# Performance work log

Hardware: AMD Instinct MI355X
Metric: run time of the kernel (lower is better)

Reference implementation:

```python
import jax, jax.numpy as jnp
import numpy as np
import math

B, L, DIM = 2, 2048, 1024
NUM_HEADS, QUANTUM_HEADS, CHUNK = 16, 2, 64
HD = DIM // NUM_HEADS  # 64 == CHUNK (required by the original broadcast)
TH = NUM_HEADS - QUANTUM_HEADS
STEPS = 2048
LN_EPS = 1e-5


def setup_inputs() -> dict:
    key = jax.random.key(0)
    ks = jax.random.split(key, 12)
    inp = {
        'x': jax.random.normal(ks[0], (B, L, DIM), dtype=jnp.float32),
        # to_quantum_state: Linear(HD, 2HD) + LayerNorm(2HD) + Tanh
        'wq1': jax.random.normal(ks[1], (HD, 2 * HD), dtype=jnp.float32) * 0.05,
        'bq1': jnp.zeros((2 * HD,), dtype=jnp.float32),
        'ln_g': jnp.ones((2 * HD,), dtype=jnp.float32),
        'ln_b': jnp.zeros((2 * HD,), dtype=jnp.float32),
        'phase_shifts': jax.random.normal(ks[2], (QUANTUM_HEADS,), dtype=jnp.float32) * 0.02,
        'freqs': jax.random.normal(ks[3], (QUANTUM_HEADS,), dtype=jnp.float32) * 0.02,
        # traditional heads: q/k/v projections, no bias
        'wq': jax.random.normal(ks[4], (DIM, TH * HD), dtype=jnp.float32) * 0.02,
        'wk': jax.random.normal(ks[5], (DIM, TH * HD), dtype=jnp.float32) * 0.02,
        'wv': jax.random.normal(ks[6], (DIM, TH * HD), dtype=jnp.float32) * 0.02,
        # output projection
        'wo': jax.random.normal(ks[7], (DIM, DIM), dtype=jnp.float32) * 0.02,
        'bo': jnp.zeros((DIM,), dtype=jnp.float32),
    }
    return inp


def _quantum_state(t, wq1, bq1, ln_g, ln_b):
    # Linear -> LayerNorm -> Tanh; split into (amp, phase)
    h = t @ wq1 + bq1
    mu = h.mean(-1, keepdims=True)
    var = ((h - mu) ** 2).mean(-1, keepdims=True)
    h = (h - mu) * jax.lax.rsqrt(var + LN_EPS) * ln_g + ln_b
    h = jnp.tanh(h)
    return h[..., :HD], h[..., HD:]


def reference(x, wq1, bq1, ln_g, ln_b, phase_shifts, freqs, wq, wk, wv, wo, bo):
    two_pi = 2.0 * math.pi
    angles = jnp.linspace(0.0, two_pi, STEPS)  # torch.linspace is endpoint-inclusive
    cos_table = jnp.cos(angles)
    inv_sqrt_hd = 1.0 / math.sqrt(HD)
    nc = L // CHUNK

    quantum_outs = []
    for h in range(QUANTUM_HEADS):
        xh = x[..., h * HD:(h + 1) * HD]                       # [B,L,HD]
        amp, phase = _quantum_state(xh, wq1, bq1, ln_g, ln_b)  # each [B,L,HD]
        qa = amp.reshape(B, nc, CHUNK, HD)
        qp = phase.reshape(B, nc, CHUNK, HD)
        # keys/values are truncated to the FIRST `chunk` tokens (original quirk)
        ka = amp[:, :CHUNK]        # [B,CHUNK,HD]
        kp = phase[:, :CHUNK]
        v = xh[:, :CHUNK]
        # phase_diff[b,c,i,j] = qp[b,c,i,j] - kp[b,j,i]  (needs CHUNK == HD)
        pd = (qp - jnp.swapaxes(kp, -1, -2)[:, None]) * freqs[h] + phase_shifts[h]
        idx = jnp.mod(pd / two_pi * STEPS, STEPS).astype(jnp.int32)  # in [0, STEPS)
        interference = cos_table[idx]                          # [B,nc,CHUNK,CHUNK]
        scores = jnp.einsum('bcih,bjh->bcij', qa, ka) * interference
        attn = jax.nn.softmax(scores * inv_sqrt_hd, axis=-1)
        out = jnp.einsum('bcij,bjh->bcih', attn, v).reshape(B, L, HD)
        quantum_outs.append(out)

    # traditional multi-head attention on full x
    q = (x @ wq).reshape(B, L, TH, HD)
    k = (x @ wk).reshape(B, L, TH, HD)
    vv = (x @ wv).reshape(B, L, TH, HD)
    scores = jnp.einsum('bqhd,bkhd->bhqk', q, k) * inv_sqrt_hd
    attn = jax.nn.softmax(scores, axis=-1)
    trad = jnp.einsum('bhqk,bkhd->bqhd', attn, vv).reshape(B, L, TH * HD)

    out = jnp.concatenate(quantum_outs + [trad], axis=-1)  # [B,L,DIM]
    return out @ wo + bo
```

## Files before the change

kernel.cpp:

```cpp
#include <hip/hip_runtime.h>
#include <hip/hip_bf16.h>
#include <math.h>

#define B_ 2
#define L_ 2048
#define DIM_ 1024
#define HD_ 64
#define TH_ 14
#define TWO_PI_F 6.28318530717958647692f
#define QSCALE_F 0.1803368801111204f

typedef __bf16 bf16_t;
typedef __bf16 bf16x8 __attribute__((ext_vector_type(8)));
typedef __bf16 bf16x4 __attribute__((ext_vector_type(4)));
typedef float f32x4 __attribute__((ext_vector_type(4)));
typedef float f32x16 __attribute__((ext_vector_type(16)));
typedef unsigned int u32x2 __attribute__((ext_vector_type(2)));

static __device__ __forceinline__ bf16_t f2b(float f) { return (bf16_t)f; }

static __device__ __forceinline__ float fexp2(float x) {
#if __has_builtin(__builtin_amdgcn_exp2f)
  return __builtin_amdgcn_exp2f(x);
#else
  return exp2f(x);
#endif
}

static __device__ __forceinline__ unsigned int cvtpk(float a, float b) {
  unsigned int r;
  asm("v_cvt_pk_bf16_f32 %0, %1, %2" : "=v"(r) : "v"(a), "v"(b));
  return r;
}

static __device__ __forceinline__ void gl16(const bf16_t* g, bf16_t* l) {
  __builtin_amdgcn_global_load_lds(
      (const __attribute__((address_space(1))) void*)g,
      (__attribute__((address_space(3))) void*)l, 16, 0, 0);
}

static __device__ __forceinline__ void swap32(unsigned int& a, unsigned int& b) {
#if __has_builtin(__builtin_amdgcn_permlane32_swap)
  u32x2 r = __builtin_amdgcn_permlane32_swap(a, b, false, false);
  a = r[0];
  b = r[1];
#else
  const int l = (int)(threadIdx.x & 63);
  unsigned int bp_a = (unsigned int)__builtin_amdgcn_ds_bpermute((l ^ 32) << 2, (int)a);
  unsigned int bp_b = (unsigned int)__builtin_amdgcn_ds_bpermute((l ^ 32) << 2, (int)b);
  unsigned int na = (l < 32) ? a : bp_b;
  unsigned int nb = (l < 32) ? bp_a : b;
  a = na;
  b = nb;
#endif
}

__global__ __launch_bounds__(256)
void k_prep(const float* __restrict__ x, const float* __restrict__ wq1,
            const float* __restrict__ bq1, const float* __restrict__ ln_g,
            const float* __restrict__ ln_b, const float* __restrict__ wq,
            const float* __restrict__ wk, const float* __restrict__ wv,
            const float* __restrict__ wo, bf16_t* __restrict__ xb,
            bf16_t* __restrict__ wt_qkv, bf16_t* __restrict__ wt_o,
            bf16_t* __restrict__ amp_b, float* __restrict__ phase) {
  __shared__ float tile[32][33];
  const int t = threadIdx.x;
  const int bid = blockIdx.x;
  if (bid < 4096) {
    const int i = bid * 256 + t;
    const float4 v4 = ((const float4*)x)[i];
    bf16x4 o = {f2b(v4.x), f2b(v4.y), f2b(v4.z), f2b(v4.w)};
    *(bf16x4*)(xb + 4 * (size_t)i) = o;
  } else if (bid < 7808) {
    const float* W;
    bf16_t* Wt;
    int N, kt, nt;
    if (bid < 6784) {
      int r = bid - 4096;
      const int which = r / 896;
      r -= which * 896;
      W = (which == 0) ? wq : (which == 1) ? wk : wv;
      Wt = wt_qkv + (size_t)which * 896 * 1024;
      N = 896;
      kt = r & 31;
      nt = r >> 5;
    } else {
      const int r = bid - 6784;
      W = wo;
      Wt = wt_o;
      N = 1024;
      kt = r & 31;
      nt = r >> 5;
    }
    const int tx = t & 31, ty = t >> 5;
    const int k0 = kt * 32, n0 = nt * 32;
    #pragma unroll
    for (int i = 0; i < 4; ++i)
      tile[ty + 8 * i][tx] = W[(size_t)(k0 + ty + 8 * i) * N + n0 + tx];
    __syncthreads();
    #pragma unroll
    for (int i = 0; i < 4; ++i)
      Wt[(size_t)(n0 + ty + 8 * i) * 1024 + k0 + tx] = f2b(tile[tx][ty + 8 * i]);
  } else {
    const int gw = ((bid - 7808) * 256 + t) >> 6;
    const int lane = t & 63;
    const int h = gw >> 12;
    const int bl = gw & 4095;
    const float xv = x[(size_t)bl * DIM_ + h * HD_ + lane];
    float acc0 = bq1[lane];
    float acc1 = bq1[64 + lane];
    #pragma unroll 16
    for (int kk = 0; kk < 64; ++kk) {
      const float xk = __shfl(xv, kk, 64);
      acc0 = fmaf(xk, wq1[kk * 128 + lane], acc0);
      acc1 = fmaf(xk, wq1[kk * 128 + 64 + lane], acc1);
    }
    float s = acc0 + acc1;
    #pragma unroll
    for (int off = 32; off > 0; off >>= 1) s += __shfl_xor(s, off, 64);
    const float mu = s * (1.0f / 128.0f);
    const float d0 = acc0 - mu, d1 = acc1 - mu;
    float vsum = d0 * d0 + d1 * d1;
    #pragma unroll
    for (int off = 32; off > 0; off >>= 1) vsum += __shfl_xor(vsum, off, 64);
    const float rstd = rsqrtf(vsum * (1.0f / 128.0f) + 1e-5f);
    const float av = tanhf(d0 * rstd * ln_g[lane] + ln_b[lane]);
    const float pv = tanhf(d1 * rstd * ln_g[64 + lane] + ln_b[64 + lane]);
    const size_t o = ((size_t)h * (B_ * L_) + bl) * HD_ + lane;
    amp_b[o] = f2b(av);
    phase[o] = pv;
  }
}

__global__ __launch_bounds__(256)
void k_mm1q(const bf16_t* __restrict__ A, const bf16_t* __restrict__ Wt,
            bf16_t* __restrict__ qb, bf16_t* __restrict__ kb, bf16_t* __restrict__ vb,
            const bf16_t* __restrict__ amp_b, const float* __restrict__ phase,
            const float* __restrict__ shifts, const float* __restrict__ freqs,
            bf16_t* __restrict__ catb) {
  __shared__ char smem[32768];
  const int t = threadIdx.x;
  const int lane = t & 63, w = t >> 6;
  const int bid = blockIdx.x;
  const int v = (bid & 7) * 100 + (bid >> 3);
  if (v < 672) {
    bf16_t* Asm = (bf16_t*)smem;
    bf16_t* Bsm = (bf16_t*)(smem + 16384);
    const int wm = w >> 1, wn = w & 1;
    const int l15 = lane & 15, g = lane >> 4;
    const int m0 = (v & 31) * 128;
    const int n0 = (v >> 5) * 128;
    f32x4 acc[4][4] = {};
    for (int k0 = 0; k0 < 1024; k0 += 64) {
      __syncthreads();
      #pragma unroll
      for (int qc = 0; qc < 4; ++qc) {
        const int idx = t + 256 * qc;
        const int r = idx >> 3, cb = idx & 7;
        const int c = (cb ^ (r & 7)) * 8;
        gl16(A + (size_t)(m0 + r) * 1024 + k0 + c, Asm + w * 512 + qc * 2048);
        gl16(Wt + (size_t)(n0 + r) * 1024 + k0 + c, Bsm + w * 512 + qc * 2048);
      }
      __syncthreads();
      #pragma unroll
      for (int ks = 0; ks < 2; ++ks) {
        bf16x8 af[4], bfr[4];
        #pragma unroll
        for (int mi = 0; mi < 4; ++mi) {
          const int row = wm * 64 + mi * 16 + l15;
          af[mi] = *(const bf16x8*)((char*)Asm + row * 128 + (((ks * 4 + g) ^ (row & 7)) << 4));
        }
        #pragma unroll
        for (int ni = 0; ni < 4; ++ni) {
          const int row = wn * 64 + ni * 16 + l15;
          bfr[ni] = *(const bf16x8*)((char*)Bsm + row * 128 + (((ks * 4 + g) ^ (row & 7)) << 4));
        }
        #pragma unroll
        for (int mi = 0; mi < 4; ++mi)
          #pragma unroll
          for (int ni = 0; ni < 4; ++ni)
            acc[mi][ni] = __builtin_amdgcn_mfma_f32_16x16x32_bf16(bfr[ni], af[mi], acc[mi][ni], 0, 0, 0);
      }
    }
    const int n0w = n0 + wn * 64;
    const int which = (n0 >= 1792) ? 2 : (n0 >= 896) ? 1 : 0;
    #pragma unroll
    for (int mi = 0; mi < 4; ++mi) {
      const int m = m0 + wm * 64 + mi * 16 + (lane & 15);
      const int bsel = m >> 11, ll = m & 2047;
      #pragma unroll
      for (int ni = 0; ni < 4; ++ni) {
        const int nb = n0w + ni * 16 + (lane >> 4) * 4;
        const int nn = nb - which * 896;
        const int head = nn >> 6, hd = nn & 63;
        if (which == 2) {
          #pragma unroll
          for (int r = 0; r < 4; ++r)
            vb[(((size_t)bsel * TH_ + head) * HD_ + hd + r) * L_ + ll] = f2b(acc[mi][ni][r]);
        } else {
          const float sc = (which == 0) ? QSCALE_F : 1.0f;
          bf16_t* dst = (which == 0) ? qb : kb;
          bf16x4 pk;
          #pragma unroll
          for (int r = 0; r < 4; ++r) pk[r] = f2b(acc[mi][ni][r] * sc);
          *(bf16x4*)(dst + (((size_t)bsel * TH_ + head) * L_ + ll) * HD_ + hd) = pk;
        }
      }
    }
  } else {
    bf16_t* Kam = (bf16_t*)smem;
    bf16_t* Vt  = (bf16_t*)(smem + 8192);
    bf16_t* Ps  = (bf16_t*)(smem + 16384);
    const int l15 = lane & 15, g = lane >> 4;
    const int qv = v - 672;
    const int c = qv & 31;
    const int hb = qv >> 5;
    const int b = hb & 1;
    const int h = hb >> 1;
    const size_t abase = ((size_t)h * B_ + b) * L_ * HD_;

    {
      const int r0 = t >> 3, cb0 = t & 7;
      const int r1 = r0 + 32;
      gl16(amp_b + abase + r0 * 64 + (cb0 ^ (r0 & 7)) * 8, Kam + w * 512);
      gl16(amp_b + abase + r1 * 64 + (cb0 ^ (r1 & 7)) * 8, Kam + w * 512 + 2048);
    }
    {
      const int vj = t >> 2;
      const int vd0 = (t & 3) * 16;
      const bf16x8 va = *(const bf16x8*)(A + ((size_t)b * L_ + vj) * DIM_ + h * 64 + vd0);
      const bf16x8 vb2 = *(const bf16x8*)(A + ((size_t)b * L_ + vj) * DIM_ + h * 64 + vd0 + 8);
      #pragma unroll
      for (int e = 0; e < 8; ++e) {
        int d = vd0 + e;
        *(bf16_t*)((char*)Vt + d * 128 + (((vj >> 3) ^ (d & 7)) << 4) + (vj & 7) * 2) = va[e];
        d = vd0 + 8 + e;
        *(bf16_t*)((char*)Vt + d * 128 + (((vj >> 3) ^ (d & 7)) << 4) + (vj & 7) * 2) = vb2[e];
      }
    }
    __syncthreads();

    bf16x8 qf[2];
    {
      const size_t ro = abase + (size_t)(c * 64 + 16 * w + l15) * 64 + g * 8;
      qf[0] = *(const bf16x8*)(amp_b + ro);
      qf[1] = *(const bf16x8*)(amp_b + ro + 32);
    }
    f32x4 s[4] = {};
    #pragma unroll
    for (int ks = 0; ks < 2; ++ks) {
      #pragma unroll
      for (int nt = 0; nt < 4; ++nt) {
        const int jr = nt * 16 + l15;
        const bf16x8 kf = *(const bf16x8*)((char*)Kam + jr * 128 + (((ks * 4 + g) ^ (jr & 7)) << 4));
        s[nt] = __builtin_amdgcn_mfma_f32_16x16x32_bf16(qf[ks], kf, s[nt], 0, 0, 0);
      }
    }
    const float freq = freqs[h], shift = shifts[h];
    char* PsW = (char*)Ps + w * 2048;
    float l_acc[4];
    #pragma unroll
    for (int r = 0; r < 4; ++r) {
      const int i_loc = 16 * w + 4 * g + r;
      const float* qrow = phase + abase + (size_t)(c * 64 + i_loc) * 64;
      const float* krow = phase + abase + i_loc;
      const int row = g * 4 + r;
      float ls = 0.0f;
      #pragma unroll
      for (int nt = 0; nt < 4; ++nt) {
        const int j = nt * 16 + l15;
        const float qp = qrow[j];
        const float kp = krow[j * 64];
        const float pd = (qp - kp) * freq + shift;
        const float t1 = pd * (2048.0f / TWO_PI_F);
        float mm = fmodf(t1, 2048.0f);
        if (mm < 0.0f) mm += 2048.0f;
        int idx = (int)mm;
        idx = idx > 2047 ? 2047 : idx;
        const float interf = cosf((float)idx * (TWO_PI_F / 2047.0f));
        const float sc = s[nt][r] * interf * 0.125f;
        const float e = expf(sc);
        ls += e;
        *(bf16_t*)(PsW + row * 128 + (((j >> 3) ^ (row & 7)) << 4) + (j & 7) * 2) = f2b(e);
      }
      #pragma unroll
      for (int off = 1; off < 16; off <<= 1) ls += __shfl_xor(ls, off, 64);
      l_acc[r] = ls;
    }
    f32x4 o[4] = {};
    #pragma unroll
    for (int ks = 0; ks < 2; ++ks) {
      const bf16x8 pa = *(const bf16x8*)(PsW + l15 * 128 + (((ks * 4 + g) ^ (l15 & 7)) << 4));
      #pragma unroll
      for (int nt = 0; nt < 4; ++nt) {
        const int dr = nt * 16 + l15;
        const bf16x8 vf = *(const bf16x8*)((char*)Vt + dr * 128 + (((ks * 4 + g) ^ (dr & 7)) << 4));
        o[nt] = __builtin_amdgcn_mfma_f32_16x16x32_bf16(pa, vf, o[nt], 0, 0, 0);
      }
    }
    #pragma unroll
    for (int r = 0; r < 4; ++r) {
      const float inv = 1.0f / l_acc[r];
      const int qrow = c * 64 + 16 * w + g * 4 + r;
      #pragma unroll
      for (int nt = 0; nt < 4; ++nt)
        catb[((size_t)b * L_ + qrow) * DIM_ + h * 64 + nt * 16 + l15] = f2b(o[nt][r] * inv);
    }
  }
}

__global__ __launch_bounds__(256)
void k_mm0(const bf16_t* __restrict__ A, const bf16_t* __restrict__ Wt,
           const float* __restrict__ bias, float* __restrict__ outf) {
  __shared__ bf16_t Asm[128 * 64];
  __shared__ bf16_t Bsm[128 * 64];
  const int t = threadIdx.x;
  const int lane = t & 63, w = t >> 6;
  const int wm = w >> 1, wn = w & 1;
  const int l15 = lane & 15, g = lane >> 4;
  const int bid = blockIdx.x;
  const int v = (bid & 7) * 32 + (bid >> 3);
  const int m0 = (v & 31) * 128;
  const int n0 = (v >> 5) * 128;
  f32x4 acc[4][4] = {};
  for (int k0 = 0; k0 < 1024; k0 += 64) {
    __syncthreads();
    #pragma unroll
    for (int qc = 0; qc < 4; ++qc) {
      const int idx = t + 256 * qc;
      const int r = idx >> 3, cb = idx & 7;
      const int c = (cb ^ (r & 7)) * 8;
      gl16(A + (size_t)(m0 + r) * 1024 + k0 + c, Asm + w * 512 + qc * 2048);
      gl16(Wt + (size_t)(n0 + r) * 1024 + k0 + c, Bsm + w * 512 + qc * 2048);
    }
    __syncthreads();
    #pragma unroll
    for (int ks = 0; ks < 2; ++ks) {
      bf16x8 af[4], bfr[4];
      #pragma unroll
      for (int mi = 0; mi < 4; ++mi) {
        const int row = wm * 64 + mi * 16 + l15;
        af[mi] = *(const bf16x8*)((char*)Asm + row * 128 + (((ks * 4 + g) ^ (row & 7)) << 4));
      }
      #pragma unroll
      for (int ni = 0; ni < 4; ++ni) {
        const int row = wn * 64 + ni * 16 + l15;
        bfr[ni] = *(const bf16x8*)((char*)Bsm + row * 128 + (((ks * 4 + g) ^ (row & 7)) << 4));
      }
      #pragma unroll
      for (int mi = 0; mi < 4; ++mi)
        #pragma unroll
        for (int ni = 0; ni < 4; ++ni)
          acc[mi][ni] = __builtin_amdgcn_mfma_f32_16x16x32_bf16(bfr[ni], af[mi], acc[mi][ni], 0, 0, 0);
    }
  }
  #pragma unroll
  for (int mi = 0; mi < 4; ++mi) {
    const int m = m0 + wm * 64 + mi * 16 + l15;
    #pragma unroll
    for (int ni = 0; ni < 4; ++ni) {
      const int nb = n0 + wn * 64 + ni * 16 + g * 4;
      const float4 bv = *(const float4*)&bias[nb];
      float4 r4;
      r4.x = acc[mi][ni][0] + bv.x;
      r4.y = acc[mi][ni][1] + bv.y;
      r4.z = acc[mi][ni][2] + bv.z;
      r4.w = acc[mi][ni][3] + bv.w;
      *(float4*)&outf[(size_t)m * 1024 + nb] = r4;
    }
  }
}

__global__ __launch_bounds__(256)
void k_flash2(const bf16_t* __restrict__ qg, const bf16_t* __restrict__ kg,
              const bf16_t* __restrict__ vt, bf16_t* __restrict__ catb) {
  __shared__ bf16_t Ks2[2][64 * 64];
  __shared__ bf16_t Vs2[2][64 * 64];
  const int t = threadIdx.x;
  const int lane = t & 63, w = t >> 6;
  const int l31 = lane & 31, hi = lane >> 5;
  int bid = blockIdx.x;
  bid = (bid & 7) * 56 + (bid >> 3);
  const int qblk = bid & 15, bh = bid >> 4;
  const int head = bh % TH_, b = bh / TH_;
  const size_t base = (size_t)bh * (L_ * HD_);
  const int q = qblk * 128 + w * 32 + l31;
  const int r0 = t >> 3, cb0 = t & 7;
  const int r1 = r0 + 32;
  const int c0 = (cb0 ^ (r0 & 7)) * 8;
  const int c1 = (cb0 ^ (r1 & 7)) * 8;
  const int ubase = w * 512;

  bf16x8 qf[4];
  #pragma unroll
  for (int slot = 0; slot < 4; ++slot)
    qf[slot] = *(const bf16x8*)(qg + base + (size_t)q * 64 + 16 * slot + 8 * hi);

  f32x16 oT[2] = {};
  float l_acc = 0.0f;

  {
    const bf16_t* ksrc = kg + base;
    const bf16_t* vsrc = vt + base;
    gl16(ksrc + r0 * 64 + c0, &Ks2[0][ubase]);
    gl16(ksrc + r1 * 64 + c1, &Ks2[0][ubase + 2048]);
    gl16(vsrc + (size_t)r0 * L_ + c0, &Vs2[0][ubase]);
    gl16(vsrc + (size_t)r1 * L_ + c1, &Vs2[0][ubase + 2048]);
  }
  for (int kt = 0; kt < 32; ++kt) {
    const int cur = kt & 1;
    if (kt < 31) {
      const bf16_t* ksrc = kg + base + (size_t)(kt + 1) * 64 * 64;
      const bf16_t* vsrc = vt + base + (kt + 1) * 64;
      bf16_t* kd = &Ks2[cur ^ 1][0];
      bf16_t* vd = &Vs2[cur ^ 1][0];
      gl16(ksrc + r0 * 64 + c0, kd + ubase);
      gl16(ksrc + r1 * 64 + c1, kd + ubase + 2048);
      gl16(vsrc + (size_t)r0 * L_ + c0, vd + ubase);
      gl16(vsrc + (size_t)r1 * L_ + c1, vd + ubase + 2048);
      asm volatile("s_waitcnt vmcnt(4)" ::: "memory");
    } else {
      asm volatile("s_waitcnt vmcnt(0)" ::: "memory");
    }
    __builtin_amdgcn_sched_barrier(0);
    __builtin_amdgcn_s_barrier();
    const char* Kc = (const char*)&Ks2[cur][0];
    const char* Vc = (const char*)&Vs2[cur][0];
    f32x16 sT0 = {}, sT1 = {};
    __builtin_amdgcn_s_setprio(1);
    #pragma unroll
    for (int slot = 0; slot < 4; ++slot) {
      const int row0 = l31;
      const int row1 = 32 + l31;
      const bf16x8 kf0 = *(const bf16x8*)(Kc + row0 * 128 + (((2 * slot + hi) ^ (row0 & 7)) << 4));
      const bf16x8 kf1 = *(const bf16x8*)(Kc + row1 * 128 + (((2 * slot + hi) ^ (row1 & 7)) << 4));
      sT0 = __builtin_amdgcn_mfma_f32_32x32x16_bf16(kf0, qf[slot], sT0, 0, 0, 0);
      sT1 = __builtin_amdgcn_mfma_f32_32x32x16_bf16(kf1, qf[slot], sT1, 0, 0, 0);
    }
    __builtin_amdgcn_s_setprio(0);
    unsigned int W0[8], W1[8];
    float la = 0.0f;
    #pragma unroll
    for (int rp = 0; rp < 8; ++rp) {
      const float p00 = fexp2(sT0[2 * rp]);
      const float p01 = fexp2(sT0[2 * rp + 1]);
      const float p10 = fexp2(sT1[2 * rp]);
      const float p11 = fexp2(sT1[2 * rp + 1]);
      la += (p00 + p01) + (p10 + p11);
      W0[rp] = cvtpk(p00, p01);
      W1[rp] = cvtpk(p10, p11);
    }
    l_acc += la;
    unsigned int pb[4][4];
    #pragma unroll
    for (int m1 = 0; m1 < 2; ++m1) {
      unsigned int u, vv;
      u = W0[m1];     vv = W0[2 + m1]; swap32(u, vv); pb[0][m1] = u; pb[0][m1 + 2] = vv;
      u = W0[4 + m1]; vv = W0[6 + m1]; swap32(u, vv); pb[1][m1] = u; pb[1][m1 + 2] = vv;
      u = W1[m1];     vv = W1[2 + m1]; swap32(u, vv); pb[2][m1] = u; pb[2][m1 + 2] = vv;
      u = W1[4 + m1]; vv = W1[6 + m1]; swap32(u, vv); pb[3][m1] = u; pb[3][m1 + 2] = vv;
    }
    __builtin_amdgcn_s_setprio(1);
    #pragma unroll
    for (int slot = 0; slot < 4; ++slot) {
      union { unsigned int u[4]; bf16x8 v8; } pf;
      pf.u[0] = pb[slot][0]; pf.u[1] = pb[slot][1];
      pf.u[2] = pb[slot][2]; pf.u[3] = pb[slot][3];
      #pragma unroll
      for (int dt = 0; dt < 2; ++dt) {
        const int row = 32 * dt + l31;
        const bf16x8 vf = *(const bf16x8*)(Vc + row * 128 + (((2 * slot + hi) ^ (row & 7)) << 4));
        oT[dt] = __builtin_amdgcn_mfma_f32_32x32x16_bf16(vf, pf.v8, oT[dt], 0, 0, 0);
      }
    }
    __builtin_amdgcn_s_setprio(0);
    __builtin_amdgcn_s_barrier();
  }
  const float l_tot = l_acc + __shfl_xor(l_acc, 32, 64);
  const float inv = 1.0f / l_tot;
  const size_t obase = ((size_t)b * L_ + q) * DIM_ + 128 + head * 64;
  #pragma unroll
  for (int dt = 0; dt < 2; ++dt) {
    #pragma unroll
    for (int rq = 0; rq < 4; ++rq) {
      bf16x4 pk;
      #pragma unroll
      for (int e = 0; e < 4; ++e) pk[e] = f2b(oT[dt][4 * rq + e] * inv);
      *(bf16x4*)(catb + obase + 32 * dt + 8 * rq + 4 * hi) = pk;
    }
  }
}

extern "C" void kernel_launch(void* const* d_in, const int* in_sizes, int n_in,
                              void* d_out, int out_size, void* d_ws, size_t ws_size,
                              hipStream_t stream) {
  (void)in_sizes; (void)n_in; (void)out_size; (void)ws_size;
  const float* x      = (const float*)d_in[0];
  const float* wq1    = (const float*)d_in[1];
  const float* bq1    = (const float*)d_in[2];
  const float* ln_g   = (const float*)d_in[3];
  const float* ln_b   = (const float*)d_in[4];
  const float* shifts = (const float*)d_in[5];
  const float* freqs  = (const float*)d_in[6];
  const float* wq     = (const float*)d_in[7];
  const float* wk     = (const float*)d_in[8];
  const float* wv     = (const float*)d_in[9];
  const float* wo     = (const float*)d_in[10];
  const float* bo     = (const float*)d_in[11];
  float* out = (float*)d_out;

  char* p = (char*)d_ws;
  bf16_t* amp_b  = (bf16_t*)p; p += (size_t)2 * B_ * L_ * HD_ * 2;
  float* phase   = (float*)p;  p += (size_t)2 * B_ * L_ * HD_ * 4;
  bf16_t* xb     = (bf16_t*)p; p += (size_t)B_ * L_ * DIM_ * 2;
  bf16_t* wt_qkv = (bf16_t*)p; p += (size_t)2688 * 1024 * 2;
  bf16_t* wt_o   = (bf16_t*)p; p += (size_t)1024 * 1024 * 2;
  bf16_t* qb     = (bf16_t*)p; p += (size_t)B_ * TH_ * L_ * HD_ * 2;
  bf16_t* kb     = (bf16_t*)p; p += (size_t)B_ * TH_ * L_ * HD_ * 2;
  bf16_t* vtb    = (bf16_t*)p; p += (size_t)B_ * TH_ * L_ * HD_ * 2;
  bf16_t* catb   = (bf16_t*)p;

  k_prep<<<dim3(9856), dim3(256), 0, stream>>>(x, wq1, bq1, ln_g, ln_b,
                                               wq, wk, wv, wo,
                                               xb, wt_qkv, wt_o, amp_b, phase);
  k_mm1q<<<dim3(800), dim3(256), 0, stream>>>(xb, wt_qkv, qb, kb, vtb,
                                              amp_b, phase, shifts, freqs, catb);
  k_flash2<<<dim3(448), dim3(256), 0, stream>>>(qb, kb, vtb, catb);
  k_mm0<<<dim3(256), dim3(256), 0, stream>>>(catb, wt_o, bo, out);
}
```

Measured before the change: 142.0 us.

## Split flash attention key range across two wave groups per block

The flash attention kernel now launches 512 threads per block. Two groups of four waves each process half of the key tiles (16 each) for the same 128 queries, and their partial outputs and row sums are merged through shared memory at the end. The aim is to double the waves per block and halve each wave's sequential loop, improving latency hiding on 448 blocks. The cost is a 64KB shared buffer, an extra reduction pass through LDS, and possible occupancy limits from the larger block. The softmax has no running max, so plain summation of the partial results is valid.

```diff
diff --git a/kernel.cpp b/kernel.cpp
--- a/kernel.cpp
+++ b/kernel.cpp
@@ -371,25 +371,29 @@
   }
 }
 
-__global__ __launch_bounds__(256)
+__global__ __launch_bounds__(512)
 void k_flash2(const bf16_t* __restrict__ qg, const bf16_t* __restrict__ kg,
               const bf16_t* __restrict__ vt, bf16_t* __restrict__ catb) {
-  __shared__ bf16_t Ks2[2][64 * 64];
-  __shared__ bf16_t Vs2[2][64 * 64];
+  __shared__ char smem[65536];
   const int t = threadIdx.x;
   const int lane = t & 63, w = t >> 6;
+  const int g2 = w >> 2, wl = w & 3;
   const int l31 = lane & 31, hi = lane >> 5;
   int bid = blockIdx.x;
   bid = (bid & 7) * 56 + (bid >> 3);
   const int qblk = bid & 15, bh = bid >> 4;
   const int head = bh % TH_, b = bh / TH_;
   const size_t base = (size_t)bh * (L_ * HD_);
-  const int q = qblk * 128 + w * 32 + l31;
-  const int r0 = t >> 3, cb0 = t & 7;
+  const int q = qblk * 128 + wl * 32 + l31;
+  const int tl = t & 255;
+  const int r0 = tl >> 3, cb0 = tl & 7;
   const int r1 = r0 + 32;
   const int c0 = (cb0 ^ (r0 & 7)) * 8;
   const int c1 = (cb0 ^ (r1 & 7)) * 8;
-  const int ubase = w * 512;
+  const int ubase = wl * 512;
+  bf16_t* Kg = (bf16_t*)(smem + g2 * 32768);
+  bf16_t* Vg = (bf16_t*)(smem + g2 * 32768 + 16384);
+  const int kt0 = g2 * 16;
 
   bf16x8 qf[4];
   #pragma unroll
@@ -400,20 +404,20 @@
   float l_acc = 0.0f;
 
   {
-    const bf16_t* ksrc = kg + base;
-    const bf16_t* vsrc = vt + base;
-    gl16(ksrc + r0 * 64 + c0, &Ks2[0][ubase]);
-    gl16(ksrc + r1 * 64 + c1, &Ks2[0][ubase + 2048]);
-    gl16(vsrc + (size_t)r0 * L_ + c0, &Vs2[0][ubase]);
-    gl16(vsrc + (size_t)r1 * L_ + c1, &Vs2[0][ubase + 2048]);
-  }
-  for (int kt = 0; kt < 32; ++kt) {
+    const bf16_t* ksrc = kg + base + (size_t)kt0 * 64 * 64;
+    const bf16_t* vsrc = vt + base + kt0 * 64;
+    gl16(ksrc + r0 * 64 + c0, Kg + ubase);
+    gl16(ksrc + r1 * 64 + c1, Kg + ubase + 2048);
+    gl16(vsrc + (size_t)r0 * L_ + c0, Vg + ubase);
+    gl16(vsrc + (size_t)r1 * L_ + c1, Vg + ubase + 2048);
+  }
+  for (int kt = 0; kt < 16; ++kt) {
     const int cur = kt & 1;
-    if (kt < 31) {
-      const bf16_t* ksrc = kg + base + (size_t)(kt + 1) * 64 * 64;
-      const bf16_t* vsrc = vt + base + (kt + 1) * 64;
-      bf16_t* kd = &Ks2[cur ^ 1][0];
-      bf16_t* vd = &Vs2[cur ^ 1][0];
+    if (kt < 15) {
+      const bf16_t* ksrc = kg + base + (size_t)(kt0 + kt + 1) * 64 * 64;
+      const bf16_t* vsrc = vt + base + (kt0 + kt + 1) * 64;
+      bf16_t* kd = Kg + (cur ^ 1) * 4096;
+      bf16_t* vd = Vg + (cur ^ 1) * 4096;
       gl16(ksrc + r0 * 64 + c0, kd + ubase);
       gl16(ksrc + r1 * 64 + c1, kd + ubase + 2048);
       gl16(vsrc + (size_t)r0 * L_ + c0, vd + ubase);
@@ -424,8 +428,8 @@
     }
     __builtin_amdgcn_sched_barrier(0);
     __builtin_amdgcn_s_barrier();
-    const char* Kc = (const char*)&Ks2[cur][0];
-    const char* Vc = (const char*)&Vs2[cur][0];
+    const char* Kc = (const char*)(Kg + cur * 4096);
+    const char* Vc = (const char*)(Vg + cur * 4096);
     f32x16 sT0 = {}, sT1 = {};
     __builtin_amdgcn_s_setprio(1);
     #pragma unroll
@@ -476,17 +480,34 @@
     __builtin_amdgcn_s_setprio(0);
     __builtin_amdgcn_s_barrier();
   }
-  const float l_tot = l_acc + __shfl_xor(l_acc, 32, 64);
-  const float inv = 1.0f / l_tot;
-  const size_t obase = ((size_t)b * L_ + q) * DIM_ + 128 + head * 64;
-  #pragma unroll
-  for (int dt = 0; dt < 2; ++dt) {
-    #pragma unroll
-    for (int rq = 0; rq < 4; ++rq) {
-      bf16x4 pk;
-      #pragma unroll
-      for (int e = 0; e < 4; ++e) pk[e] = f2b(oT[dt][4 * rq + e] * inv);
-      *(bf16x4*)(catb + obase + 32 * dt + 8 * rq + 4 * hi) = pk;
+  const float l_w = l_acc + __shfl_xor(l_acc, 32, 64);
+  __syncthreads();
+  float* obuf = (float*)(smem + 32768);
+  float* lbuf = (float*)smem;
+  if (g2 == 1) {
+    #pragma unroll
+    for (int dt = 0; dt < 2; ++dt)
+      #pragma unroll
+      for (int e = 0; e < 16; ++e)
+        obuf[(dt * 16 + e) * 256 + wl * 64 + lane] = oT[dt][e];
+    lbuf[wl * 64 + lane] = l_w;
+  }
+  __syncthreads();
+  if (g2 == 0) {
+    const float l_tot = l_w + lbuf[wl * 64 + lane];
+    const float inv = 1.0f / l_tot;
+    const size_t obase = ((size_t)b * L_ + q) * DIM_ + 128 + head * 64;
+    #pragma unroll
+    for (int dt = 0; dt < 2; ++dt) {
+      #pragma unroll
+      for (int rq = 0; rq < 4; ++rq) {
+        bf16x4 pk;
+        #pragma unroll
+        for (int e = 0; e < 4; ++e)
+          pk[e] = f2b((oT[dt][4 * rq + e] +
+                       obuf[(dt * 16 + 4 * rq + e) * 256 + wl * 64 + lane]) * inv);
+        *(bf16x4*)(catb + obase + 32 * dt + 8 * rq + 4 * hi) = pk;
+      }
     }
   }
 }
@@ -525,6 +546,6 @@
                                                xb, wt_qkv, wt_o, amp_b, phase);
   k_mm1q<<<dim3(800), dim3(256), 0, stream>>>(xb, wt_qkv, qb, kb, vtb,
                                               amp_b, phase, shifts, freqs, catb);
-  k_flash2<<<dim3(448), dim3(256), 0, stream>>>(qb, kb, vtb, catb);
+  k_flash2<<<dim3(448), dim3(512), 0, stream>>>(qb, kb, vtb, catb);
   k_mm0<<<dim3(256), dim3(256), 0, stream>>>(catb, wt_o, bo, out);
 }
```

Result: faster. 129.7 us (-8.7%).
